# Kernel optimization log

Hardware: AMD Instinct MI355X
Metric: run time of the kernel (lower is better)

The kernel has to match this reference:

```python
import jax, jax.numpy as jnp
import numpy as np

MARGIN = 1.0
EPS = 1e-12


def setup_inputs() -> dict:
    key = jax.random.key(0)
    k1, k2 = jax.random.split(key)
    embeddings = jax.random.normal(k1, (4096, 768), dtype=jnp.float32)
    labels = jax.random.randint(k2, (4096,), 0, 4, dtype=jnp.int64)
    return {"embeddings": embeddings, "labels": labels}


def reference(embeddings, labels):
    # F.normalize(p=2, dim=1): x / max(||x||, eps)
    norm = jnp.linalg.norm(embeddings, axis=1, keepdims=True)
    e = embeddings / jnp.maximum(norm, EPS)

    # Euclidean pairwise distance matrix (not squared)
    dot = e @ e.T                                  # [N, N]
    sq = jnp.diagonal(dot)                         # [N]
    dist = sq[None, :] - 2.0 * dot + sq[:, None]
    dist = jnp.sqrt(jnp.maximum(dist, 0.0) + EPS)  # [N, N]

    # Masks: positives = same label, off-diagonal; negatives = different label
    n = labels.shape[0]
    eq = labels[None, :] == labels[:, None]
    pos_mask = eq & ~jnp.eye(n, dtype=bool)
    neg_mask = ~eq

    # Batch-hard mining: per-anchor hardest positive (masked max) and
    # hardest negative (masked min) -- replaces the per-row Python loop.
    d_ap = jnp.max(jnp.where(pos_mask, dist, -jnp.inf), axis=1)  # [N]
    d_an = jnp.min(jnp.where(neg_mask, dist, jnp.inf), axis=1)   # [N]

    valid = jnp.any(pos_mask, axis=1)  # anchors with at least one positive
    per_anchor = jnp.maximum(d_ap - d_an + MARGIN, 0.0)
    per_anchor = jnp.where(valid, per_anchor, 0.0)
    n_valid = jnp.maximum(jnp.sum(valid.astype(jnp.float32)), 1.0)
    return jnp.sum(per_anchor) / n_valid
```

## Files before the change

kernel.cpp:

```cpp
#include <hip/hip_runtime.h>
#include <math.h>

#define N 4096
#define D 768
#define MARGIN 1.0f

typedef _Float16 half8 __attribute__((ext_vector_type(8)));
typedef float f32x4 __attribute__((ext_vector_type(4)));

__device__ __forceinline__ void gl2lds16(const void* g, void* l) {
    __builtin_amdgcn_global_load_lds((const __attribute__((address_space(1))) void*)g,
                                     (__attribute__((address_space(3))) void*)l, 16, 0, 0);
}

__global__ __launch_bounds__(256) void normalize_kernel(const float* __restrict__ x,
                                                        _Float16* __restrict__ e,
                                                        float* __restrict__ sq,
                                                        unsigned* __restrict__ ap_bits,
                                                        unsigned* __restrict__ an_bits) {
    const int row = blockIdx.x;
    const int tid = threadIdx.x;
    const float* xr = x + (size_t)row * D;
    _Float16* er = e + (size_t)row * D;

    float v0 = xr[tid];
    float v1 = xr[tid + 256];
    float v2 = xr[tid + 512];
    float s = v0 * v0 + v1 * v1 + v2 * v2;

    #pragma unroll
    for (int off = 32; off; off >>= 1) s += __shfl_down(s, off, 64);

    __shared__ float wsum[4];
    if ((tid & 63) == 0) wsum[tid >> 6] = s;
    __syncthreads();
    float tot = wsum[0] + wsum[1] + wsum[2] + wsum[3];

    float norm = sqrtf(tot);
    float scale = 1.0f / fmaxf(norm, 1e-12f);

    er[tid]       = (_Float16)(v0 * scale);
    er[tid + 256] = (_Float16)(v1 * scale);
    er[tid + 512] = (_Float16)(v2 * scale);
    if (tid == 0) {
        sq[row] = tot * scale * scale;
        ap_bits[row] = 0u;
        an_bits[row] = 0x7f800000u;
    }
}

__global__ __launch_bounds__(256) void mine_kernel(const _Float16* __restrict__ e,
                                                   const float* __restrict__ sq,
                                                   const int* __restrict__ labels,
                                                   unsigned* __restrict__ ap_bits,
                                                   unsigned* __restrict__ an_bits) {
    __shared__ unsigned short S[8192];

    int bi = 0, rem = blockIdx.x;
    while (rem >= 32 - bi) { rem -= 32 - bi; ++bi; }
    const int bj = bi + rem;
    const int i0 = bi * 128, j0 = bj * 128;

    const int tid  = threadIdx.x;
    const int w    = tid >> 6;
    const int lane = tid & 63;
    const int wi   = (w & 1) * 64;
    const int wj   = (w >> 1) * 64;
    const int ln15 = lane & 15;
    const int lq   = lane >> 4;

    f32x4 acc[4][4] = {};

    for (int k0 = 0; k0 < D; k0 += 32) {
        #pragma unroll
        for (int p = 0; p < 2; ++p) {
            int s  = p * 256 + tid;
            int r  = s >> 2;
            int kg = (s & 3) ^ ((r >> 1) & 3);
            const _Float16* ga = e + (size_t)(i0 + r) * D + k0 + kg * 8;
            const _Float16* gb = e + (size_t)(j0 + r) * D + k0 + kg * 8;
            char* la = (char*)S + (p * 256 + w * 64) * 16;
            char* lb = (char*)S + 8192 + (p * 256 + w * 64) * 16;
            gl2lds16(ga, la);
            gl2lds16(gb, lb);
        }
        __syncthreads();

        half8 af[4], bf[4];
        #pragma unroll
        for (int mt = 0; mt < 4; ++mt) {
            int r  = wi + mt * 16 + ln15;
            int kx = lq ^ ((r >> 1) & 3);
            af[mt] = *(const half8*)&S[r * 32 + kx * 8];
        }
        #pragma unroll
        for (int nt = 0; nt < 4; ++nt) {
            int r  = wj + nt * 16 + ln15;
            int kx = lq ^ ((r >> 1) & 3);
            bf[nt] = *(const half8*)&S[4096 + r * 32 + kx * 8];
        }
        #pragma unroll
        for (int mt = 0; mt < 4; ++mt)
            #pragma unroll
            for (int nt = 0; nt < 4; ++nt)
                acc[mt][nt] = __builtin_amdgcn_mfma_f32_16x16x32_f16(af[mt], bf[nt], acc[mt][nt], 0, 0, 0);
        __syncthreads();
    }

    float sqi[4][4]; int labi[4][4];
    #pragma unroll
    for (int mt = 0; mt < 4; ++mt)
        #pragma unroll
        for (int rg = 0; rg < 4; ++rg) {
            int i = i0 + wi + mt * 16 + lq * 4 + rg;
            sqi[mt][rg] = sq[i];
            labi[mt][rg] = labels[i];
        }
    float sqj[4]; int labj[4];
    #pragma unroll
    for (int nt = 0; nt < 4; ++nt) {
        int j = j0 + wj + nt * 16 + ln15;
        sqj[nt] = sq[j];
        labj[nt] = labels[j];
    }

    float api[4][4], ani[4][4], apj[4], anj[4];
    #pragma unroll
    for (int mt = 0; mt < 4; ++mt)
        #pragma unroll
        for (int rg = 0; rg < 4; ++rg) { api[mt][rg] = -INFINITY; ani[mt][rg] = INFINITY; }
    #pragma unroll
    for (int nt = 0; nt < 4; ++nt) { apj[nt] = -INFINITY; anj[nt] = INFINITY; }

    #pragma unroll
    for (int nt = 0; nt < 4; ++nt) {
        int j = j0 + wj + nt * 16 + ln15;
        #pragma unroll
        for (int mt = 0; mt < 4; ++mt)
            #pragma unroll
            for (int rg = 0; rg < 4; ++rg) {
                int i = i0 + wi + mt * 16 + lq * 4 + rg;
                float d2 = sqi[mt][rg] + sqj[nt] - 2.0f * acc[mt][nt][rg];
                float dist = sqrtf(fmaxf(d2, 0.0f) + 1e-12f);
                if (labi[mt][rg] == labj[nt]) {
                    if (i != j) {
                        api[mt][rg] = fmaxf(api[mt][rg], dist);
                        apj[nt]     = fmaxf(apj[nt], dist);
                    }
                } else {
                    ani[mt][rg] = fminf(ani[mt][rg], dist);
                    anj[nt]     = fminf(anj[nt], dist);
                }
            }
    }

    #pragma unroll
    for (int mt = 0; mt < 4; ++mt)
        #pragma unroll
        for (int rg = 0; rg < 4; ++rg) {
            float a_ = api[mt][rg], n_ = ani[mt][rg];
            #pragma unroll
            for (int off = 1; off < 16; off <<= 1) {
                a_ = fmaxf(a_, __shfl_xor(a_, off, 64));
                n_ = fminf(n_, __shfl_xor(n_, off, 64));
            }
            if (ln15 == 0) {
                int i = i0 + wi + mt * 16 + lq * 4 + rg;
                if (a_ > -1.0e37f) atomicMax(&ap_bits[i], __float_as_uint(a_));
                if (n_ <  1.0e37f) atomicMin(&an_bits[i], __float_as_uint(n_));
            }
        }

    if (bi != bj) {
        #pragma unroll
        for (int nt = 0; nt < 4; ++nt) {
            float a_ = apj[nt], n_ = anj[nt];
            #pragma unroll
            for (int off = 16; off < 64; off <<= 1) {
                a_ = fmaxf(a_, __shfl_xor(a_, off, 64));
                n_ = fminf(n_, __shfl_xor(n_, off, 64));
            }
            if (lq == 0) {
                int j = j0 + wj + nt * 16 + ln15;
                if (a_ > -1.0e37f) atomicMax(&ap_bits[j], __float_as_uint(a_));
                if (n_ <  1.0e37f) atomicMin(&an_bits[j], __float_as_uint(n_));
            }
        }
    }
}

__global__ __launch_bounds__(256) void finalize_kernel(const unsigned* __restrict__ ap_bits,
                                                       const unsigned* __restrict__ an_bits,
                                                       const int* __restrict__ labels,
                                                       float* __restrict__ out) {
    __shared__ int cnt[4];
    __shared__ float red[8];
    int tid = threadIdx.x;
    if (tid < 4) cnt[tid] = 0;
    __syncthreads();

    int local[4] = {0, 0, 0, 0};
    for (int i = tid; i < N; i += 256) local[labels[i] & 3]++;
    #pragma unroll
    for (int c = 0; c < 4; c++) atomicAdd(&cnt[c], local[c]);
    __syncthreads();

    float sum = 0.f, nv = 0.f;
    for (int i = tid; i < N; i += 256) {
        int l = labels[i] & 3;
        if (cnt[l] >= 2) {
            nv += 1.f;
            float apv = __uint_as_float(ap_bits[i]);
            float anv = __uint_as_float(an_bits[i]);
            if (anv < 3.0e38f) sum += fmaxf(apv - anv + MARGIN, 0.f);
        }
    }

    #pragma unroll
    for (int off = 32; off; off >>= 1) {
        sum += __shfl_down(sum, off, 64);
        nv  += __shfl_down(nv,  off, 64);
    }
    int w = tid >> 6;
    if ((tid & 63) == 0) { red[w] = sum; red[4 + w] = nv; }
    __syncthreads();
    if (tid == 0) {
        float s = red[0] + red[1] + red[2] + red[3];
        float n = red[4] + red[5] + red[6] + red[7];
        out[0] = s / fmaxf(n, 1.f);
    }
}

extern "C" void kernel_launch(void* const* d_in, const int* in_sizes, int n_in,
                              void* d_out, int out_size, void* d_ws, size_t ws_size,
                              hipStream_t stream) {
    const float* x = (const float*)d_in[0];
    const int* labels = (const int*)d_in[1];
    float* out = (float*)d_out;

    _Float16* e = (_Float16*)d_ws;
    float* sq = (float*)(e + (size_t)N * D);
    unsigned* ap_bits = (unsigned*)(sq + N);
    unsigned* an_bits = ap_bits + N;

    normalize_kernel<<<N, 256, 0, stream>>>(x, e, sq, ap_bits, an_bits);
    mine_kernel<<<528, 256, 0, stream>>>(e, sq, labels, ap_bits, an_bits);
    finalize_kernel<<<1, 256, 0, stream>>>(ap_bits, an_bits, labels, out);
}
```

Baseline: 135.9 us.

## Double-buffer GEMM LDS loads, wave-per-row normalize, fuse finalize via last-block counter

The mine kernel now double-buffers its LDS tiles so the next k-slice is prefetched while the current one feeds MFMA, which removes one barrier per iteration. The normalize kernel processes one row per wave with float4 loads and half4 stores, and launches a quarter as many blocks. The finalize kernel is folded into the mine kernel through an atomic completion counter, so the last block does the reduction and one launch is saved. The cost is doubled LDS per block, which may lower occupancy, plus an atomic counter and fences at the end of every block.

```diff
diff --git a/kernel.cpp b/kernel.cpp
--- a/kernel.cpp
+++ b/kernel.cpp
@@ -4,8 +4,10 @@
 #define N 4096
 #define D 768
 #define MARGIN 1.0f
+#define NBLK 528
 
 typedef _Float16 half8 __attribute__((ext_vector_type(8)));
+typedef _Float16 half4 __attribute__((ext_vector_type(4)));
 typedef float f32x4 __attribute__((ext_vector_type(4)));
 
 __device__ __forceinline__ void gl2lds16(const void* g, void* l) {
@@ -17,44 +19,49 @@
                                                         _Float16* __restrict__ e,
                                                         float* __restrict__ sq,
                                                         unsigned* __restrict__ ap_bits,
-                                                        unsigned* __restrict__ an_bits) {
-    const int row = blockIdx.x;
+                                                        unsigned* __restrict__ an_bits,
+                                                        unsigned* __restrict__ counter) {
     const int tid = threadIdx.x;
-    const float* xr = x + (size_t)row * D;
-    _Float16* er = e + (size_t)row * D;
-
-    float v0 = xr[tid];
-    float v1 = xr[tid + 256];
-    float v2 = xr[tid + 512];
-    float s = v0 * v0 + v1 * v1 + v2 * v2;
-
-    #pragma unroll
-    for (int off = 32; off; off >>= 1) s += __shfl_down(s, off, 64);
-
-    __shared__ float wsum[4];
-    if ((tid & 63) == 0) wsum[tid >> 6] = s;
-    __syncthreads();
-    float tot = wsum[0] + wsum[1] + wsum[2] + wsum[3];
-
-    float norm = sqrtf(tot);
-    float scale = 1.0f / fmaxf(norm, 1e-12f);
-
-    er[tid]       = (_Float16)(v0 * scale);
-    er[tid + 256] = (_Float16)(v1 * scale);
-    er[tid + 512] = (_Float16)(v2 * scale);
-    if (tid == 0) {
-        sq[row] = tot * scale * scale;
+    const int wave = tid >> 6, lane = tid & 63;
+    const int row = blockIdx.x * 4 + wave;
+
+    const float4* xr = (const float4*)(x + (size_t)row * D);
+    float4 f0 = xr[lane];
+    float4 f1 = xr[lane + 64];
+    float4 f2 = xr[lane + 128];
+
+    float s = f0.x*f0.x + f0.y*f0.y + f0.z*f0.z + f0.w*f0.w
+            + f1.x*f1.x + f1.y*f1.y + f1.z*f1.z + f1.w*f1.w
+            + f2.x*f2.x + f2.y*f2.y + f2.z*f2.z + f2.w*f2.w;
+    #pragma unroll
+    for (int off = 1; off < 64; off <<= 1) s += __shfl_xor(s, off, 64);
+
+    float scale = 1.0f / fmaxf(sqrtf(s), 1e-12f);
+
+    half4* er = (half4*)(e + (size_t)row * D);
+    half4 h0 = { (_Float16)(f0.x*scale), (_Float16)(f0.y*scale), (_Float16)(f0.z*scale), (_Float16)(f0.w*scale) };
+    half4 h1 = { (_Float16)(f1.x*scale), (_Float16)(f1.y*scale), (_Float16)(f1.z*scale), (_Float16)(f1.w*scale) };
+    half4 h2 = { (_Float16)(f2.x*scale), (_Float16)(f2.y*scale), (_Float16)(f2.z*scale), (_Float16)(f2.w*scale) };
+    er[lane]       = h0;
+    er[lane + 64]  = h1;
+    er[lane + 128] = h2;
+
+    if (lane == 0) {
+        sq[row] = s * scale * scale;
         ap_bits[row] = 0u;
         an_bits[row] = 0x7f800000u;
     }
+    if (blockIdx.x == 0 && tid == 0) *counter = 0u;
 }
 
 __global__ __launch_bounds__(256) void mine_kernel(const _Float16* __restrict__ e,
                                                    const float* __restrict__ sq,
                                                    const int* __restrict__ labels,
                                                    unsigned* __restrict__ ap_bits,
-                                                   unsigned* __restrict__ an_bits) {
-    __shared__ unsigned short S[8192];
+                                                   unsigned* __restrict__ an_bits,
+                                                   unsigned* __restrict__ counter,
+                                                   float* __restrict__ out) {
+    __shared__ unsigned short S[16384];
 
     int bi = 0, rem = blockIdx.x;
     while (rem >= 32 - bi) { rem -= 32 - bi; ++bi; }
@@ -71,40 +78,46 @@
 
     f32x4 acc[4][4] = {};
 
-    for (int k0 = 0; k0 < D; k0 += 32) {
+    auto stage = [&](int k0, int buf) {
         #pragma unroll
         for (int p = 0; p < 2; ++p) {
-            int s  = p * 256 + tid;
-            int r  = s >> 2;
-            int kg = (s & 3) ^ ((r >> 1) & 3);
+            int sIdx = p * 256 + tid;
+            int r  = sIdx >> 2;
+            int kg = (sIdx & 3) ^ ((r >> 1) & 3);
             const _Float16* ga = e + (size_t)(i0 + r) * D + k0 + kg * 8;
             const _Float16* gb = e + (size_t)(j0 + r) * D + k0 + kg * 8;
-            char* la = (char*)S + (p * 256 + w * 64) * 16;
-            char* lb = (char*)S + 8192 + (p * 256 + w * 64) * 16;
+            char* base = (char*)S + buf * 16384;
+            char* la = base + (p * 256 + w * 64) * 16;
+            char* lb = base + 8192 + (p * 256 + w * 64) * 16;
             gl2lds16(ga, la);
             gl2lds16(gb, lb);
         }
+    };
+
+    stage(0, 0);
+    for (int kt = 0; kt < 24; ++kt) {
         __syncthreads();
-
+        if (kt + 1 < 24) stage((kt + 1) * 32, (kt + 1) & 1);
+
+        const int bb = (kt & 1) * 8192;
         half8 af[4], bf[4];
         #pragma unroll
         for (int mt = 0; mt < 4; ++mt) {
             int r  = wi + mt * 16 + ln15;
             int kx = lq ^ ((r >> 1) & 3);
-            af[mt] = *(const half8*)&S[r * 32 + kx * 8];
+            af[mt] = *(const half8*)&S[bb + r * 32 + kx * 8];
         }
         #pragma unroll
         for (int nt = 0; nt < 4; ++nt) {
             int r  = wj + nt * 16 + ln15;
             int kx = lq ^ ((r >> 1) & 3);
-            bf[nt] = *(const half8*)&S[4096 + r * 32 + kx * 8];
+            bf[nt] = *(const half8*)&S[bb + 4096 + r * 32 + kx * 8];
         }
         #pragma unroll
         for (int mt = 0; mt < 4; ++mt)
             #pragma unroll
             for (int nt = 0; nt < 4; ++nt)
                 acc[mt][nt] = __builtin_amdgcn_mfma_f32_16x16x32_f16(af[mt], bf[nt], acc[mt][nt], 0, 0, 0);
-        __syncthreads();
     }
 
     float sqi[4][4]; int labi[4][4];
@@ -187,18 +200,18 @@
             }
         }
     }
-}
-
-__global__ __launch_bounds__(256) void finalize_kernel(const unsigned* __restrict__ ap_bits,
-                                                       const unsigned* __restrict__ an_bits,
-                                                       const int* __restrict__ labels,
-                                                       float* __restrict__ out) {
+
+    __shared__ unsigned lastFlag;
     __shared__ int cnt[4];
     __shared__ float red[8];
-    int tid = threadIdx.x;
+    __threadfence();
+    if (tid == 0) lastFlag = (atomicAdd(counter, 1u) == NBLK - 1) ? 1u : 0u;
+    __syncthreads();
+    if (!lastFlag) return;
+    __threadfence();
+
     if (tid < 4) cnt[tid] = 0;
     __syncthreads();
-
     int local[4] = {0, 0, 0, 0};
     for (int i = tid; i < N; i += 256) local[labels[i] & 3]++;
     #pragma unroll
@@ -210,8 +223,8 @@
         int l = labels[i] & 3;
         if (cnt[l] >= 2) {
             nv += 1.f;
-            float apv = __uint_as_float(ap_bits[i]);
-            float anv = __uint_as_float(an_bits[i]);
+            float apv = __uint_as_float(atomicAdd(&ap_bits[i], 0u));
+            float anv = __uint_as_float(atomicAdd(&an_bits[i], 0u));
             if (anv < 3.0e38f) sum += fmaxf(apv - anv + MARGIN, 0.f);
         }
     }
@@ -221,8 +234,7 @@
         sum += __shfl_down(sum, off, 64);
         nv  += __shfl_down(nv,  off, 64);
     }
-    int w = tid >> 6;
-    if ((tid & 63) == 0) { red[w] = sum; red[4 + w] = nv; }
+    if ((tid & 63) == 0) { red[tid >> 6] = sum; red[4 + (tid >> 6)] = nv; }
     __syncthreads();
     if (tid == 0) {
         float s = red[0] + red[1] + red[2] + red[3];
@@ -242,8 +254,8 @@
     float* sq = (float*)(e + (size_t)N * D);
     unsigned* ap_bits = (unsigned*)(sq + N);
     unsigned* an_bits = ap_bits + N;
-
-    normalize_kernel<<<N, 256, 0, stream>>>(x, e, sq, ap_bits, an_bits);
-    mine_kernel<<<528, 256, 0, stream>>>(e, sq, labels, ap_bits, an_bits);
-    finalize_kernel<<<1, 256, 0, stream>>>(ap_bits, an_bits, labels, out);
-}
+    unsigned* counter = an_bits + N;
+
+    normalize_kernel<<<N / 4, 256, 0, stream>>>(x, e, sq, ap_bits, an_bits, counter);
+    mine_kernel<<<NBLK, 256, 0, stream>>>(e, sq, labels, ap_bits, an_bits, counter, out);
+}
```

Result: slower. 143.7 us (+5.7%).
